# Kernel tuning notes

Hardware: AMD Instinct MI355X
Metric: run time of the kernel (lower is better)

Reference implementation:

```python
import jax, jax.numpy as jnp
import numpy as np

EPS = 1e-7
MAX_NORM = 1.0 - 1e-5  # Poincare ball (c=1) projection radius
NUM_NODES = 50000
NUM_EDGES = 800000
NUM_GRAPHS = 512
D_IN = 64
D_H = 64
D_OUT = 16


def _norm(x):
    return jnp.clip(jnp.linalg.norm(x, axis=-1, keepdims=True), EPS)


def expmap0(u):
    n = _norm(u)
    return jnp.tanh(n) * u / n


def logmap0(x):
    n = _norm(x)
    nc = jnp.clip(n, EPS, MAX_NORM)
    return jnp.arctanh(nc) * x / n


def proj(x):
    n = _norm(x)
    return jnp.where(n > MAX_NORM, x * (MAX_NORM / n), x)


def mobius_add(x, y):
    x2 = jnp.sum(x * x, axis=-1, keepdims=True)
    y2 = jnp.sum(y * y, axis=-1, keepdims=True)
    xy = jnp.sum(x * y, axis=-1, keepdims=True)
    num = (1.0 + 2.0 * xy + y2) * x + (1.0 - x2) * y
    den = jnp.clip(1.0 + 2.0 * xy + x2 * y2, EPS)
    return num / den


def hyp_linear(x, W, b):
    # mobius matvec + hyperbolic bias add
    h = proj(expmap0(logmap0(x) @ W.T))
    hb = proj(expmap0(b))
    return proj(mobius_add(h, hb))


def hyp_agg(x, src, dst, num_nodes):
    # mean aggregation of neighbor messages in the tangent space at the origin
    xt = logmap0(x)                                   # [N, d]
    msg = xt[src]                                     # [E, d] gather
    s = jax.ops.segment_sum(msg, dst, num_segments=num_nodes)
    cnt = jax.ops.segment_sum(jnp.ones((msg.shape[0],), xt.dtype), dst,
                              num_segments=num_nodes)
    agg = s / jnp.clip(cnt, 1.0)[:, None]
    return proj(expmap0(agg))


def hyp_act(x, act):
    return proj(expmap0(act(logmap0(x))))


def hgcn_layer(x, W, b, src, dst, num_nodes, act):
    h = hyp_linear(x, W, b)
    h = hyp_agg(h, src, dst, num_nodes)
    if act is not None:
        h = hyp_act(h, act)
    return h


def setup_inputs() -> dict:
    key = jax.random.key(0)
    ks = jax.random.split(key, 12)
    x = jax.random.normal(ks[0], (NUM_NODES, D_IN), jnp.float32) * 0.1
    edge_index = jax.random.randint(ks[1], (2, NUM_EDGES), 0, NUM_NODES, jnp.int64 if jax.config.jax_enable_x64 else jnp.int32)
    batch = jnp.sort(jax.random.randint(ks[2], (NUM_NODES,), 0, NUM_GRAPHS))
    def w(k, o, i):
        return jax.random.normal(k, (o, i), jnp.float32) * (1.0 / np.sqrt(i))
    return {
        "x": x,
        "W1": w(ks[3], D_H, D_IN), "b1": jnp.zeros((D_H,), jnp.float32),
        "W2": w(ks[4], D_H, D_H),  "b2": jnp.zeros((D_H,), jnp.float32),
        "W3": w(ks[5], D_H, D_H),  "b3": jnp.zeros((D_H,), jnp.float32),
        "W4": w(ks[6], D_OUT, D_H), "b4": jnp.zeros((D_OUT,), jnp.float32),
        "edge_index": edge_index,
        "batch": batch,
    }


def reference(x, W1, b1, W2, b2, W3, b3, W4, b4, edge_index, batch):
    act = lambda v: jax.nn.leaky_relu(v, 0.2)
    n = x.shape[0]
    src, dst = edge_index[0], edge_index[1]
    h = proj(expmap0(x))
    h = hgcn_layer(h, W1, b1, src, dst, n, act)
    h = hgcn_layer(h, W2, b2, src, dst, n, act)
    h = hgcn_layer(h, W3, b3, src, dst, n, None)
    t = logmap0(h)
    # global mean pool over graphs (eval-mode dropout = identity)
    s = jax.ops.segment_sum(t, batch, num_segments=NUM_GRAPHS)
    cnt = jax.ops.segment_sum(jnp.ones((n,), t.dtype), batch, num_segments=NUM_GRAPHS)
    pooled = s / jnp.clip(cnt, 1.0)[:, None]            # [G, d]
    h = proj(expmap0(pooled))
    out = hyp_linear(h, W4, b4)                          # HNNLayer, no activation
    return out
```

## Files before the change

### kernel.cpp

```cpp
#include <hip/hip_runtime.h>
#include <hip/hip_fp16.h>

#define EPSF 1e-7f
#define MAXNORM (1.0f - 1e-5f)

__device__ __forceinline__ float rsum64(float v) {
#pragma unroll
  for (int m = 32; m; m >>= 1) v += __shfl_xor(v, m, 64);
  return v;
}
__device__ __forceinline__ float rsum16(float v) {
#pragma unroll
  for (int m = 8; m; m >>= 1) v += __shfl_xor(v, m, 64);
  return v;
}
__device__ __forceinline__ float gr8(float v) {
  v += __shfl_xor(v, 1, 64);
  v += __shfl_xor(v, 2, 64);
  v += __shfl_xor(v, 4, 64);
  return v;
}

__device__ __forceinline__ float frcp(float x) { return __builtin_amdgcn_rcpf(x); }
__device__ __forceinline__ float fsqrt_(float x) { return __builtin_amdgcn_sqrtf(x); }
__device__ __forceinline__ float tanh_fast(float x) {
  x = fminf(x, 20.f);
  float e = __builtin_amdgcn_exp2f(x * 2.88539008178f);
  return (e - 1.f) * frcp(e + 1.f);
}
__device__ __forceinline__ float atanh_fast(float x) {
  return 0.34657359028f * __builtin_amdgcn_logf((1.f + x) * frcp(1.f - x));
}
__device__ __forceinline__ float lp_exp_log_scale(float nu) {
  float te = tanh_fast(nu);
  float tec = fminf(fmaxf(te, EPSF), MAXNORM);
  return atanh_fast(tec) * frcp(fmaxf(te, EPSF)) * te * frcp(nu);
}

__device__ __forceinline__ float4 ld4(const float* p) {
  return *reinterpret_cast<const float4*>(p);
}

__device__ __forceinline__ void gather8h(const unsigned short* __restrict__ csr,
                                         const __half* __restrict__ xtp,
                                         int r0, int deg, int g, int sub,
                                         float acc[8]) {
  const uint4* xt4 = reinterpret_cast<const uint4*>(xtp);
  for (int j0 = 0; j0 < deg; j0 += 8) {
    int myidx = 0;
    if (j0 + sub < deg) myidx = (int)csr[r0 + j0 + sub];
#pragma unroll
    for (int m = 0; m < 8; ++m) {
      int idx = __shfl(myidx, (g << 3) | m, 64);
      float msk = (j0 + m < deg) ? 1.f : 0.f;
      union { uint4 u; __half2 h[4]; } U;
      U.u = xt4[(size_t)idx * 8 + sub];
      float2 f0 = __half22float2(U.h[0]);
      float2 f1 = __half22float2(U.h[1]);
      float2 f2 = __half22float2(U.h[2]);
      float2 f3 = __half22float2(U.h[3]);
      acc[0] = fmaf(msk, f0.x, acc[0]); acc[1] = fmaf(msk, f0.y, acc[1]);
      acc[2] = fmaf(msk, f1.x, acc[2]); acc[3] = fmaf(msk, f1.y, acc[3]);
      acc[4] = fmaf(msk, f2.x, acc[4]); acc[5] = fmaf(msk, f2.y, acc[5]);
      acc[6] = fmaf(msk, f3.x, acc[6]); acc[7] = fmaf(msk, f3.y, acc[7]);
    }
  }
}

__device__ __forceinline__ void st8h(__half* __restrict__ xt, int node, int sub,
                                     const float o[8]) {
  union { uint4 u; __half2 h[4]; } U;
  U.h[0] = __floats2half2_rn(o[0], o[1]);
  U.h[1] = __floats2half2_rn(o[2], o[3]);
  U.h[2] = __floats2half2_rn(o[4], o[5]);
  U.h[3] = __floats2half2_rn(o[6], o[7]);
  reinterpret_cast<uint4*>(xt)[(size_t)node * 8 + sub] = U.u;
}

__device__ __forceinline__ void linear_tail8(
    const float* __restrict__ Wl, float* __restrict__ sc, int g, int sub,
    int lane, const float t2[8], const float hb8[8], float hb2, float out8[8]) {
  float4* sw = reinterpret_cast<float4*>(sc + g * 68 + sub * 8);
  sw[0] = make_float4(t2[0], t2[1], t2[2], t2[3]);
  sw[1] = make_float4(t2[4], t2[5], t2[6], t2[7]);
  float y[8] = {0.f, 0.f, 0.f, 0.f, 0.f, 0.f, 0.f, 0.f};
  const float4* Wrow = reinterpret_cast<const float4*>(Wl + lane * 68);
#pragma unroll
  for (int q = 0; q < 16; ++q) {
    float4 w = Wrow[q];
#pragma unroll
    for (int g2 = 0; g2 < 8; ++g2) {
      float4 tq = *reinterpret_cast<const float4*>(sc + g2 * 68 + q * 4);
      y[g2] = fmaf(w.x, tq.x, fmaf(w.y, tq.y, fmaf(w.z, tq.z, fmaf(w.w, tq.w, y[g2]))));
    }
  }
#pragma unroll
  for (int g2 = 0; g2 < 8; ++g2) sc[g2 * 68 + lane] = y[g2];
  float4 r0 = *reinterpret_cast<const float4*>(sc + g * 68 + sub * 8);
  float4 r1 = *reinterpret_cast<const float4*>(sc + g * 68 + sub * 8 + 4);
  float yv[8] = {r0.x, r0.y, r0.z, r0.w, r1.x, r1.y, r1.z, r1.w};
  float p1 = 0.f, p2 = 0.f;
#pragma unroll
  for (int j = 0; j < 8; ++j) {
    p1 = fmaf(yv[j], yv[j], p1);
    p2 = fmaf(yv[j], hb8[j], p2);
  }
  p1 = gr8(p1); p2 = gr8(p2);
  float ny = fmaxf(fsqrt_(p1), EPSF);
  float cy = fminf(tanh_fast(ny), MAXNORM);
  float k = cy * frcp(ny);
  float xy = k * p2;
  float x2 = cy * cy;
  float aa = 1.f + 2.f * xy + hb2;
  float cc = 1.f - x2;
  float den = fmaxf(1.f + 2.f * xy + x2 * hb2, EPSF);
  float rd = frcp(den);
  float nr2 = (aa * aa * x2 + 2.f * aa * cc * xy + cc * cc * hb2) * rd * rd;
  float nr = fmaxf(fsqrt_(nr2), EPSF);
  float s = atanh_fast(fminf(nr, MAXNORM)) * frcp(nr);
  float sk = s * rd;
#pragma unroll
  for (int j = 0; j < 8; ++j) out8[j] = sk * (aa * k * yv[j] + cc * hb8[j]);
}

__global__ void k_hist8(const int* __restrict__ dst, int* __restrict__ deg8,
                        int* __restrict__ rank, int E, int N) {
  int e = blockIdx.x * blockDim.x + threadIdx.x;
  if (e >= E) return;
  int c = blockIdx.x & 7;
  rank[e] = atomicAdd(&deg8[(size_t)c * N + dst[e]], 1);
}

__global__ void __launch_bounds__(256) k_red8(const int* __restrict__ deg8,
                                              int* __restrict__ offs8,
                                              int* __restrict__ deg, int N) {
  int d = blockIdx.x * blockDim.x + threadIdx.x;
  if (d >= N) return;
  int s = 0;
#pragma unroll
  for (int k = 0; k < 8; ++k) {
    int v = deg8[(size_t)k * N + d];
    offs8[(size_t)k * N + d] = s;
    s += v;
  }
  deg[d] = s;
}

__global__ void __launch_bounds__(256) k_scanA(const int* __restrict__ deg,
                                               int* __restrict__ locscan,
                                               int* __restrict__ partial, int N) {
  __shared__ int buf[256];
  int i = blockIdx.x * 256 + threadIdx.x;
  int v = (i < N) ? deg[i] : 0;
  buf[threadIdx.x] = v;
  __syncthreads();
#pragma unroll
  for (int off = 1; off < 256; off <<= 1) {
    int t = (threadIdx.x >= off) ? buf[threadIdx.x - off] : 0;
    __syncthreads();
    buf[threadIdx.x] += t;
    __syncthreads();
  }
  if (i < N) locscan[i] = buf[threadIdx.x] - v;
  if (threadIdx.x == 255) partial[blockIdx.x] = buf[255];
}

__global__ void __launch_bounds__(256) k_scanB(int* __restrict__ partial, int nb) {
  __shared__ int buf[256];
  int v = (threadIdx.x < nb) ? partial[threadIdx.x] : 0;
  buf[threadIdx.x] = v;
  __syncthreads();
#pragma unroll
  for (int off = 1; off < 256; off <<= 1) {
    int t = (threadIdx.x >= off) ? buf[threadIdx.x - off] : 0;
    __syncthreads();
    buf[threadIdx.x] += t;
    __syncthreads();
  }
  if (threadIdx.x < nb) partial[threadIdx.x] = buf[threadIdx.x] - v;
}

__global__ void __launch_bounds__(256) k_scanC(const int* __restrict__ locscan,
                                               const int* __restrict__ partial,
                                               int* __restrict__ rowptr, int N, int E) {
  int i = blockIdx.x * 256 + threadIdx.x;
  if (i < N) rowptr[i] = locscan[i] + partial[blockIdx.x];
  if (i == 0) rowptr[N] = E;
}

__global__ void k_fillnr(const int* __restrict__ src, const int* __restrict__ dst,
                         const int* __restrict__ rank,
                         const int* __restrict__ rowptr,
                         const int* __restrict__ offs8,
                         unsigned short* __restrict__ csr, int E, int N) {
  int e = blockIdx.x * blockDim.x + threadIdx.x;
  if (e >= E) return;
  int c = blockIdx.x & 7;
  int d = dst[e];
  csr[rowptr[d] + offs8[(size_t)c * N + d] + rank[e]] = (unsigned short)src[e];
}

__global__ void k_gsize(const int* __restrict__ batch, float* __restrict__ cntg,
                        int N, int G) {
  int g = blockIdx.x * blockDim.x + threadIdx.x;
  if (g >= G) return;
  int lo = 0, hi = N;
  while (lo < hi) { int mid = (lo + hi) >> 1; if (batch[mid] < g) lo = mid + 1; else hi = mid; }
  int lb = lo;
  lo = 0; hi = N; int g1 = g + 1;
  while (lo < hi) { int mid = (lo + hi) >> 1; if (batch[mid] < g1) lo = mid + 1; else hi = mid; }
  cntg[g] = (float)(lo - lb);
}

__global__ void __launch_bounds__(192) k_prepb(const float* __restrict__ b1,
                                               const float* __restrict__ b2,
                                               const float* __restrict__ b3,
                                               float* __restrict__ hb_all,
                                               float* __restrict__ hb2_all) {
  int w = threadIdx.x >> 6, lane = threadIdx.x & 63;
  const float* b = (w == 0) ? b1 : (w == 1) ? b2 : b3;
  float bb = b[lane];
  float nb = fmaxf(fsqrt_(rsum64(bb * bb)), EPSF);
  float tb = tanh_fast(nb);
  float cb = fminf(tb, MAXNORM);
  float hb = cb * frcp(nb) * bb;
  hb_all[w * 64 + lane] = hb;
  if (lane == 0) hb2_all[w] = cb * cb;
}

__global__ void __launch_bounds__(512) k_lin1(const float* __restrict__ x,
                                              const float* __restrict__ W,
                                              const float* __restrict__ hb,
                                              const float* __restrict__ hb2p,
                                              __half* __restrict__ xt, int N) {
  __shared__ __align__(16) float Wl[64 * 68];
  __shared__ __align__(16) float sc_all[8][8 * 68];
  int tid = threadIdx.x, wid = tid >> 6, lane = tid & 63;
  int g = lane >> 3, sub = lane & 7;
  for (int i = tid; i < 4096; i += 512) Wl[(i >> 6) * 68 + (i & 63)] = W[i];
  __syncthreads();
  float hb2 = hb2p[0];
  float4 h0 = ld4(hb + sub * 8), h1 = ld4(hb + sub * 8 + 4);
  float hb8[8] = {h0.x, h0.y, h0.z, h0.w, h1.x, h1.y, h1.z, h1.w};

  int slot = blockIdx.x * 64 + wid * 8 + g;
  bool valid = slot < N;
  int node = valid ? slot : 0;
  const float* row = x + (size_t)node * 64 + sub * 8;
  float4 v0 = ld4(row), v1 = ld4(row + 4);
  float xa[8] = {v0.x, v0.y, v0.z, v0.w, v1.x, v1.y, v1.z, v1.w};
  float p = 0.f;
#pragma unroll
  for (int j = 0; j < 8; ++j) p = fmaf(xa[j], xa[j], p);
  p = gr8(p);
  float na = fmaxf(fsqrt_(p), EPSF);
  float sc1 = lp_exp_log_scale(na);
  float t2[8];
#pragma unroll
  for (int j = 0; j < 8; ++j) t2[j] = sc1 * xa[j];
  float out8[8];
  linear_tail8(Wl, sc_all[wid], g, sub, lane, t2, hb8, hb2, out8);
  if (valid) st8h(xt, node, sub, out8);
}

__global__ void __launch_bounds__(512) k_gatherlin(
    const int* __restrict__ rowptr, const unsigned short* __restrict__ csr,
    const __half* __restrict__ xtp, const float* __restrict__ W,
    const float* __restrict__ hb, const float* __restrict__ hb2p,
    __half* __restrict__ xt, int N) {
  __shared__ __align__(16) float Wl[64 * 68];
  __shared__ __align__(16) float sc_all[8][8 * 68];
  int tid = threadIdx.x, wid = tid >> 6, lane = tid & 63;
  int g = lane >> 3, sub = lane & 7;
  for (int i = tid; i < 4096; i += 512) Wl[(i >> 6) * 68 + (i & 63)] = W[i];
  __syncthreads();
  float hb2 = hb2p[0];
  float4 h0 = ld4(hb + sub * 8), h1 = ld4(hb + sub * 8 + 4);
  float hb8[8] = {h0.x, h0.y, h0.z, h0.w, h1.x, h1.y, h1.z, h1.w};

  int slot = blockIdx.x * 64 + wid * 8 + g;
  bool valid = slot < N;
  int node = valid ? slot : 0;
  int r0 = rowptr[node];
  int deg = valid ? (rowptr[node + 1] - r0) : 0;
  float acc[8] = {0.f, 0.f, 0.f, 0.f, 0.f, 0.f, 0.f, 0.f};
  gather8h(csr, xtp, r0, deg, g, sub, acc);
  float rdeg = frcp(fmaxf((float)deg, 1.f));
  float u[8];
#pragma unroll
  for (int j = 0; j < 8; ++j) u[j] = acc[j] * rdeg;
  float p = 0.f, q = 0.f;
#pragma unroll
  for (int j = 0; j < 8; ++j) {
    float w = (u[j] < 0.f) ? 0.04f : 1.f;
    p = fmaf(u[j], u[j], p);
    q = fmaf(w * u[j], u[j], q);
  }
  p = gr8(p); q = gr8(q);
  float nu = fmaxf(fsqrt_(p), EPSF);
  float s1 = lp_exp_log_scale(nu);
  float nt = fmaxf(s1 * fsqrt_(q), EPSF);
  float f = lp_exp_log_scale(nt) * s1;
  float t2[8];
#pragma unroll
  for (int j = 0; j < 8; ++j) t2[j] = f * u[j] * ((u[j] < 0.f) ? 0.2f : 1.f);
  float out8[8];
  linear_tail8(Wl, sc_all[wid], g, sub, lane, t2, hb8, hb2, out8);
  if (valid) st8h(xt, node, sub, out8);
}

__global__ void __launch_bounds__(512) k_gpool(const int* __restrict__ rowptr,
                                               const unsigned short* __restrict__ csr,
                                               const __half* __restrict__ xtp,
                                               const int* __restrict__ batch,
                                               float* __restrict__ pooled, int N) {
  int tid = threadIdx.x, wid = tid >> 6, lane = tid & 63;
  int g = lane >> 3, sub = lane & 7;
  int slot = blockIdx.x * 64 + wid * 8 + g;
  bool valid = slot < N;
  int node = valid ? slot : 0;
  int r0 = rowptr[node];
  int deg = valid ? (rowptr[node + 1] - r0) : 0;
  float acc[8] = {0.f, 0.f, 0.f, 0.f, 0.f, 0.f, 0.f, 0.f};
  gather8h(csr, xtp, r0, deg, g, sub, acc);
  float rdeg = frcp(fmaxf((float)deg, 1.f));
  float u[8], p = 0.f;
#pragma unroll
  for (int j = 0; j < 8; ++j) {
    u[j] = acc[j] * rdeg;
    p = fmaf(u[j], u[j], p);
  }
  p = gr8(p);
  float nu = fmaxf(fsqrt_(p), EPSF);
  float s = lp_exp_log_scale(nu);
  float t8[8];
#pragma unroll
  for (int j = 0; j < 8; ++j) t8[j] = (valid ? s : 0.f) * u[j];
  int bs = batch[node];
  int b0 = __shfl(bs, 0, 64);
  bool uniform = __all(valid && bs == b0);
  if (uniform) {
#pragma unroll
    for (int j = 0; j < 8; ++j) {
      t8[j] += __shfl_xor(t8[j], 8, 64);
      t8[j] += __shfl_xor(t8[j], 16, 64);
      t8[j] += __shfl_xor(t8[j], 32, 64);
    }
    if (g == 0) {
#pragma unroll
      for (int j = 0; j < 8; ++j)
        atomicAdd(&pooled[(size_t)b0 * 64 + sub * 8 + j], t8[j]);
    }
  } else if (valid) {
#pragma unroll
    for (int j = 0; j < 8; ++j)
      atomicAdd(&pooled[(size_t)bs * 64 + sub * 8 + j], t8[j]);
  }
}

__global__ void __launch_bounds__(64) k_final(const float* __restrict__ pooled,
                                              const float* __restrict__ cntg,
                                              const float* __restrict__ W4,
                                              const float* __restrict__ b4,
                                              float* __restrict__ out, int G) {
  int g = blockIdx.x;
  int lane = threadIdx.x;
  float u = pooled[(size_t)g * 64 + lane] / fmaxf(cntg[g], 1.0f);
  float n = fmaxf(sqrtf(rsum64(u * u)), EPSF);
  float e = tanhf(n) * u / n;
  float ne = fmaxf(sqrtf(rsum64(e * e)), EPSF);
  if (ne > MAXNORM) e *= MAXNORM / ne;
  float nn = fmaxf(sqrtf(rsum64(e * e)), EPSF);
  float t = atanhf(fminf(nn, MAXNORM)) * e / nn;

  int row = lane & 15;
  float acc = 0.f;
#pragma unroll
  for (int k = 0; k < 64; ++k) {
    float tk = __shfl(t, k, 64);
    acc = fmaf(W4[row * 64 + k], tk, acc);
  }
  float ny = fmaxf(sqrtf(rsum16(acc * acc)), EPSF);
  float hy = tanhf(ny) * acc / ny;
  float nh = fmaxf(sqrtf(rsum16(hy * hy)), EPSF);
  if (nh > MAXNORM) hy *= MAXNORM / nh;
  float bb = b4[row];
  float nb = fmaxf(sqrtf(rsum16(bb * bb)), EPSF);
  float hb = tanhf(nb) * bb / nb;
  float nhb = fmaxf(sqrtf(rsum16(hb * hb)), EPSF);
  if (nhb > MAXNORM) hb *= MAXNORM / nhb;
  float x2 = rsum16(hy * hy);
  float y2 = rsum16(hb * hb);
  float xy = rsum16(hy * hb);
  float num = (1.f + 2.f * xy + y2) * hy + (1.f - x2) * hb;
  float den = fmaxf(1.f + 2.f * xy + x2 * y2, EPSF);
  float r = num / den;
  float nr = fmaxf(sqrtf(rsum16(r * r)), EPSF);
  if (nr > MAXNORM) r *= MAXNORM / nr;
  if (lane < 16) out[(size_t)g * 16 + lane] = r;
}

extern "C" void kernel_launch(void* const* d_in, const int* in_sizes, int n_in,
                              void* d_out, int out_size, void* d_ws, size_t ws_size,
                              hipStream_t stream) {
  const float* x  = (const float*)d_in[0];
  const float* W1 = (const float*)d_in[1];
  const float* b1 = (const float*)d_in[2];
  const float* W2 = (const float*)d_in[3];
  const float* b2 = (const float*)d_in[4];
  const float* W3 = (const float*)d_in[5];
  const float* b3 = (const float*)d_in[6];
  const float* W4 = (const float*)d_in[7];
  const float* b4 = (const float*)d_in[8];
  const int* ei   = (const int*)d_in[9];
  const int* batch = (const int*)d_in[10];

  int N = in_sizes[0] / 64;
  int E = in_sizes[9] / 2;
  int G = out_size / 16;
  const int* src = ei;
  const int* dst = ei + E;

  float* ws = (float*)d_ws;
  __half* xtA   = (__half*)ws;
  __half* xtB   = xtA + (size_t)N * 64;
  float* pooled = ws + (size_t)N * 64;
  float* cntg   = pooled + (size_t)G * 64;
  float* hb_all = cntg + G;
  float* hb2_all = hb_all + 192;
  int* ip       = (int*)(hb2_all + 4);
  int* deg8     = ip;
  int* offs8    = deg8 + (size_t)8 * N;
  int* deg      = offs8 + (size_t)8 * N;
  int* locscan  = deg + N;
  int* rowptr   = locscan + N;
  int* partial  = rowptr + N + 1;
  int* rank     = partial + 256;
  unsigned short* csr = (unsigned short*)(rank + E);
  float* out = (float*)d_out;

  int nbN = (N + 255) / 256;
  int nbE = (E + 255) / 256;
  int nb64 = (N + 63) / 64;

  hipMemsetAsync(deg8, 0, (size_t)8 * N * sizeof(int), stream);
  hipMemsetAsync(pooled, 0, (size_t)G * 64 * sizeof(float), stream);

  k_hist8<<<nbE, 256, 0, stream>>>(dst, deg8, rank, E, N);
  k_gsize<<<(G + 255) / 256, 256, 0, stream>>>(batch, cntg, N, G);
  k_red8<<<nbN, 256, 0, stream>>>(deg8, offs8, deg, N);
  k_scanA<<<nbN, 256, 0, stream>>>(deg, locscan, partial, N);
  k_scanB<<<1, 256, 0, stream>>>(partial, nbN);
  k_scanC<<<nbN, 256, 0, stream>>>(locscan, partial, rowptr, N, E);
  k_fillnr<<<nbE, 256, 0, stream>>>(src, dst, rank, rowptr, offs8, csr, E, N);

  k_prepb<<<1, 192, 0, stream>>>(b1, b2, b3, hb_all, hb2_all);

  k_lin1<<<nb64, 512, 0, stream>>>(x, W1, hb_all, hb2_all, xtA, N);
  k_gatherlin<<<nb64, 512, 0, stream>>>(rowptr, csr, xtA, W2, hb_all + 64,
                                        hb2_all + 1, xtB, N);
  k_gatherlin<<<nb64, 512, 0, stream>>>(rowptr, csr, xtB, W3, hb_all + 128,
                                        hb2_all + 2, xtA, N);
  k_gpool<<<nb64, 512, 0, stream>>>(rowptr, csr, xtA, batch, pooled, N);
  k_final<<<G, 64, 0, stream>>>(pooled, cntg, W4, b4, out, G);
}
```

Measured before the change: 185.0 us.

## Merge preprocessing kernels and compute bias in-kernel to cut launch count

Fuses the histogram with the graph-size kernel, the deg8 reduction with the local scan, and the CSR fill with the first linear layer into single launches split by block index. The separate bias-prep kernel is removed and each block now computes the hyperbolic bias itself. The CSR gather also prefetches the next batch of neighbor indices before processing the current one. This targets launch overhead and serialization across about 13 small kernels, at the cost of some repeated bias math per block and a multi-pass scanB loop.

```diff
diff --git a/kernel.cpp b/kernel.cpp
--- a/kernel.cpp
+++ b/kernel.cpp
@@ -41,17 +41,35 @@
   return *reinterpret_cast<const float4*>(p);
 }
 
+__device__ __forceinline__ void hb_from_b(const float* __restrict__ b, int sub,
+                                          float hb8[8], float& hb2) {
+  float4 b0 = ld4(b + sub * 8), b1 = ld4(b + sub * 8 + 4);
+  float bb8[8] = {b0.x, b0.y, b0.z, b0.w, b1.x, b1.y, b1.z, b1.w};
+  float p = 0.f;
+#pragma unroll
+  for (int j = 0; j < 8; ++j) p = fmaf(bb8[j], bb8[j], p);
+  p = gr8(p);
+  float nb = fmaxf(fsqrt_(p), EPSF);
+  float cb = fminf(tanh_fast(nb), MAXNORM);
+  float kb = cb * frcp(nb);
+#pragma unroll
+  for (int j = 0; j < 8; ++j) hb8[j] = kb * bb8[j];
+  hb2 = cb * cb;
+}
+
 __device__ __forceinline__ void gather8h(const unsigned short* __restrict__ csr,
                                          const __half* __restrict__ xtp,
                                          int r0, int deg, int g, int sub,
                                          float acc[8]) {
   const uint4* xt4 = reinterpret_cast<const uint4*>(xtp);
+  int lb = g << 3;
+  int cur = (sub < deg) ? (int)csr[r0 + sub] : 0;
   for (int j0 = 0; j0 < deg; j0 += 8) {
-    int myidx = 0;
-    if (j0 + sub < deg) myidx = (int)csr[r0 + j0 + sub];
+    int nj = j0 + 8;
+    int nxt = (nj + sub < deg) ? (int)csr[r0 + nj + sub] : 0;
 #pragma unroll
     for (int m = 0; m < 8; ++m) {
-      int idx = __shfl(myidx, (g << 3) | m, 64);
+      int idx = __shfl(cur, lb + m, 64);
       float msk = (j0 + m < deg) ? 1.f : 0.f;
       union { uint4 u; __half2 h[4]; } U;
       U.u = xt4[(size_t)idx * 8 + sub];
@@ -64,6 +82,7 @@
       acc[4] = fmaf(msk, f2.x, acc[4]); acc[5] = fmaf(msk, f2.y, acc[5]);
       acc[6] = fmaf(msk, f3.x, acc[6]); acc[7] = fmaf(msk, f3.y, acc[7]);
     }
+    cur = nxt;
   }
 }
 
@@ -123,36 +142,44 @@
   for (int j = 0; j < 8; ++j) out8[j] = sk * (aa * k * yv[j] + cc * hb8[j]);
 }
 
-__global__ void k_hist8(const int* __restrict__ dst, int* __restrict__ deg8,
-                        int* __restrict__ rank, int E, int N) {
-  int e = blockIdx.x * blockDim.x + threadIdx.x;
-  if (e >= E) return;
-  int c = blockIdx.x & 7;
-  rank[e] = atomicAdd(&deg8[(size_t)c * N + dst[e]], 1);
-}
-
-__global__ void __launch_bounds__(256) k_red8(const int* __restrict__ deg8,
-                                              int* __restrict__ offs8,
-                                              int* __restrict__ deg, int N) {
-  int d = blockIdx.x * blockDim.x + threadIdx.x;
-  if (d >= N) return;
-  int s = 0;
-#pragma unroll
-  for (int k = 0; k < 8; ++k) {
-    int v = deg8[(size_t)k * N + d];
-    offs8[(size_t)k * N + d] = s;
-    s += v;
-  }
-  deg[d] = s;
-}
-
-__global__ void __launch_bounds__(256) k_scanA(const int* __restrict__ deg,
-                                               int* __restrict__ locscan,
-                                               int* __restrict__ partial, int N) {
+__global__ void __launch_bounds__(256) k_histg(
+    const int* __restrict__ dst, int* __restrict__ deg8, int* __restrict__ rank,
+    int E, int N, const int* __restrict__ batch, float* __restrict__ cntg,
+    int G, int nbE) {
+  if ((int)blockIdx.x < nbE) {
+    int e = blockIdx.x * 256 + threadIdx.x;
+    if (e >= E) return;
+    int c = (e >> 8) & 7;
+    rank[e] = atomicAdd(&deg8[(size_t)c * N + dst[e]], 1);
+  } else {
+    int g = (blockIdx.x - nbE) * 256 + threadIdx.x;
+    if (g >= G) return;
+    int lo = 0, hi = N;
+    while (lo < hi) { int mid = (lo + hi) >> 1; if (batch[mid] < g) lo = mid + 1; else hi = mid; }
+    int lb = lo;
+    lo = 0; hi = N; int g1 = g + 1;
+    while (lo < hi) { int mid = (lo + hi) >> 1; if (batch[mid] < g1) lo = mid + 1; else hi = mid; }
+    cntg[g] = (float)(lo - lb);
+  }
+}
+
+__global__ void __launch_bounds__(256) k_scanAR(const int* __restrict__ deg8,
+                                                int* __restrict__ offs8,
+                                                int* __restrict__ locscan,
+                                                int* __restrict__ partial, int N) {
   __shared__ int buf[256];
   int i = blockIdx.x * 256 + threadIdx.x;
-  int v = (i < N) ? deg[i] : 0;
-  buf[threadIdx.x] = v;
+  int s = 0;
+  if (i < N) {
+#pragma unroll
+    for (int k = 0; k < 8; ++k) {
+      int v = deg8[(size_t)k * N + i];
+      offs8[(size_t)k * N + i] = s;
+      s += v;
+    }
+  }
+  int v0 = s;
+  buf[threadIdx.x] = v0;
   __syncthreads();
 #pragma unroll
   for (int off = 1; off < 256; off <<= 1) {
@@ -161,23 +188,30 @@
     buf[threadIdx.x] += t;
     __syncthreads();
   }
-  if (i < N) locscan[i] = buf[threadIdx.x] - v;
+  if (i < N) locscan[i] = buf[threadIdx.x] - v0;
   if (threadIdx.x == 255) partial[blockIdx.x] = buf[255];
 }
 
 __global__ void __launch_bounds__(256) k_scanB(int* __restrict__ partial, int nb) {
   __shared__ int buf[256];
-  int v = (threadIdx.x < nb) ? partial[threadIdx.x] : 0;
-  buf[threadIdx.x] = v;
-  __syncthreads();
-#pragma unroll
-  for (int off = 1; off < 256; off <<= 1) {
-    int t = (threadIdx.x >= off) ? buf[threadIdx.x - off] : 0;
+  int carry = 0;
+  for (int base = 0; base < nb; base += 256) {
+    int i = base + threadIdx.x;
+    int v = (i < nb) ? partial[i] : 0;
+    buf[threadIdx.x] = v;
     __syncthreads();
-    buf[threadIdx.x] += t;
+#pragma unroll
+    for (int off = 1; off < 256; off <<= 1) {
+      int t = (threadIdx.x >= off) ? buf[threadIdx.x - off] : 0;
+      __syncthreads();
+      buf[threadIdx.x] += t;
+      __syncthreads();
+    }
+    if (i < nb) partial[i] = carry + buf[threadIdx.x] - v;
+    int total = buf[255];
     __syncthreads();
-  }
-  if (threadIdx.x < nb) partial[threadIdx.x] = buf[threadIdx.x] - v;
+    carry += total;
+  }
 }
 
 __global__ void __launch_bounds__(256) k_scanC(const int* __restrict__ locscan,
@@ -188,95 +222,63 @@
   if (i == 0) rowptr[N] = E;
 }
 
-__global__ void k_fillnr(const int* __restrict__ src, const int* __restrict__ dst,
-                         const int* __restrict__ rank,
-                         const int* __restrict__ rowptr,
-                         const int* __restrict__ offs8,
-                         unsigned short* __restrict__ csr, int E, int N) {
-  int e = blockIdx.x * blockDim.x + threadIdx.x;
-  if (e >= E) return;
-  int c = blockIdx.x & 7;
-  int d = dst[e];
-  csr[rowptr[d] + offs8[(size_t)c * N + d] + rank[e]] = (unsigned short)src[e];
-}
-
-__global__ void k_gsize(const int* __restrict__ batch, float* __restrict__ cntg,
-                        int N, int G) {
-  int g = blockIdx.x * blockDim.x + threadIdx.x;
-  if (g >= G) return;
-  int lo = 0, hi = N;
-  while (lo < hi) { int mid = (lo + hi) >> 1; if (batch[mid] < g) lo = mid + 1; else hi = mid; }
-  int lb = lo;
-  lo = 0; hi = N; int g1 = g + 1;
-  while (lo < hi) { int mid = (lo + hi) >> 1; if (batch[mid] < g1) lo = mid + 1; else hi = mid; }
-  cntg[g] = (float)(lo - lb);
-}
-
-__global__ void __launch_bounds__(192) k_prepb(const float* __restrict__ b1,
-                                               const float* __restrict__ b2,
-                                               const float* __restrict__ b3,
-                                               float* __restrict__ hb_all,
-                                               float* __restrict__ hb2_all) {
-  int w = threadIdx.x >> 6, lane = threadIdx.x & 63;
-  const float* b = (w == 0) ? b1 : (w == 1) ? b2 : b3;
-  float bb = b[lane];
-  float nb = fmaxf(fsqrt_(rsum64(bb * bb)), EPSF);
-  float tb = tanh_fast(nb);
-  float cb = fminf(tb, MAXNORM);
-  float hb = cb * frcp(nb) * bb;
-  hb_all[w * 64 + lane] = hb;
-  if (lane == 0) hb2_all[w] = cb * cb;
-}
-
-__global__ void __launch_bounds__(512) k_lin1(const float* __restrict__ x,
-                                              const float* __restrict__ W,
-                                              const float* __restrict__ hb,
-                                              const float* __restrict__ hb2p,
-                                              __half* __restrict__ xt, int N) {
+__global__ void __launch_bounds__(512) k_filllin(
+    const int* __restrict__ src, const int* __restrict__ dst,
+    const int* __restrict__ rank, const int* __restrict__ rowptr,
+    const int* __restrict__ offs8, unsigned short* __restrict__ csr,
+    int E, int N, int nbF,
+    const float* __restrict__ x, const float* __restrict__ W,
+    const float* __restrict__ b, __half* __restrict__ xt) {
+  __shared__ __align__(16) float Wl[64 * 68];
+  __shared__ __align__(16) float sc_all[8][8 * 68];
+  if ((int)blockIdx.x < nbF) {
+    int e = blockIdx.x * 512 + threadIdx.x;
+    if (e >= E) return;
+    int c = (e >> 8) & 7;
+    int d = dst[e];
+    csr[rowptr[d] + offs8[(size_t)c * N + d] + rank[e]] = (unsigned short)src[e];
+    return;
+  }
+  int bb = blockIdx.x - nbF;
+  int tid = threadIdx.x, wid = tid >> 6, lane = tid & 63;
+  int g = lane >> 3, sub = lane & 7;
+  for (int i = tid; i < 4096; i += 512) Wl[(i >> 6) * 68 + (i & 63)] = W[i];
+  __syncthreads();
+  float hb8[8], hb2;
+  hb_from_b(b, sub, hb8, hb2);
+
+  int slot = bb * 64 + wid * 8 + g;
+  bool valid = slot < N;
+  int node = valid ? slot : 0;
+  const float* row = x + (size_t)node * 64 + sub * 8;
+  float4 v0 = ld4(row), v1 = ld4(row + 4);
+  float xa[8] = {v0.x, v0.y, v0.z, v0.w, v1.x, v1.y, v1.z, v1.w};
+  float p = 0.f;
+#pragma unroll
+  for (int j = 0; j < 8; ++j) p = fmaf(xa[j], xa[j], p);
+  p = gr8(p);
+  float na = fmaxf(fsqrt_(p), EPSF);
+  float sc1 = lp_exp_log_scale(na);
+  float t2[8];
+#pragma unroll
+  for (int j = 0; j < 8; ++j) t2[j] = sc1 * xa[j];
+  float out8[8];
+  linear_tail8(Wl, sc_all[wid], g, sub, lane, t2, hb8, hb2, out8);
+  if (valid) st8h(xt, node, sub, out8);
+}
+
+__global__ void __launch_bounds__(512) k_gatherlin(
+    const int* __restrict__ rowptr, const unsigned short* __restrict__ csr,
+    const __half* __restrict__ xtp, const float* __restrict__ W,
+    const float* __restrict__ b, __half* __restrict__ xt, int N) {
   __shared__ __align__(16) float Wl[64 * 68];
   __shared__ __align__(16) float sc_all[8][8 * 68];
   int tid = threadIdx.x, wid = tid >> 6, lane = tid & 63;
   int g = lane >> 3, sub = lane & 7;
   for (int i = tid; i < 4096; i += 512) Wl[(i >> 6) * 68 + (i & 63)] = W[i];
   __syncthreads();
-  float hb2 = hb2p[0];
-  float4 h0 = ld4(hb + sub * 8), h1 = ld4(hb + sub * 8 + 4);
-  float hb8[8] = {h0.x, h0.y, h0.z, h0.w, h1.x, h1.y, h1.z, h1.w};
-
-  int slot = blockIdx.x * 64 + wid * 8 + g;
-  bool valid = slot < N;
-  int node = valid ? slot : 0;
-  const float* row = x + (size_t)node * 64 + sub * 8;
-  float4 v0 = ld4(row), v1 = ld4(row + 4);
-  float xa[8] = {v0.x, v0.y, v0.z, v0.w, v1.x, v1.y, v1.z, v1.w};
-  float p = 0.f;
-#pragma unroll
-  for (int j = 0; j < 8; ++j) p = fmaf(xa[j], xa[j], p);
-  p = gr8(p);
-  float na = fmaxf(fsqrt_(p), EPSF);
-  float sc1 = lp_exp_log_scale(na);
-  float t2[8];
-#pragma unroll
-  for (int j = 0; j < 8; ++j) t2[j] = sc1 * xa[j];
-  float out8[8];
-  linear_tail8(Wl, sc_all[wid], g, sub, lane, t2, hb8, hb2, out8);
-  if (valid) st8h(xt, node, sub, out8);
-}
-
-__global__ void __launch_bounds__(512) k_gatherlin(
-    const int* __restrict__ rowptr, const unsigned short* __restrict__ csr,
-    const __half* __restrict__ xtp, const float* __restrict__ W,
-    const float* __restrict__ hb, const float* __restrict__ hb2p,
-    __half* __restrict__ xt, int N) {
-  __shared__ __align__(16) float Wl[64 * 68];
-  __shared__ __align__(16) float sc_all[8][8 * 68];
-  int tid = threadIdx.x, wid = tid >> 6, lane = tid & 63;
-  int g = lane >> 3, sub = lane & 7;
-  for (int i = tid; i < 4096; i += 512) Wl[(i >> 6) * 68 + (i & 63)] = W[i];
-  __syncthreads();
-  float hb2 = hb2p[0];
-  float4 h0 = ld4(hb + sub * 8), h1 = ld4(hb + sub * 8 + 4);
-  float hb8[8] = {h0.x, h0.y, h0.z, h0.w, h1.x, h1.y, h1.z, h1.w};
+  float hb8[8], hb2;
+  hb_from_b(b, sub, hb8, hb2);
 
   int slot = blockIdx.x * 64 + wid * 8 + g;
   bool valid = slot < N;
@@ -426,41 +428,33 @@
   __half* xtB   = xtA + (size_t)N * 64;
   float* pooled = ws + (size_t)N * 64;
   float* cntg   = pooled + (size_t)G * 64;
-  float* hb_all = cntg + G;
-  float* hb2_all = hb_all + 192;
-  int* ip       = (int*)(hb2_all + 4);
+  int* ip       = (int*)(cntg + G);
   int* deg8     = ip;
   int* offs8    = deg8 + (size_t)8 * N;
-  int* deg      = offs8 + (size_t)8 * N;
-  int* locscan  = deg + N;
+  int* locscan  = offs8 + (size_t)8 * N;
   int* rowptr   = locscan + N;
   int* partial  = rowptr + N + 1;
   int* rank     = partial + 256;
   unsigned short* csr = (unsigned short*)(rank + E);
   float* out = (float*)d_out;
 
+  int nbE = (E + 255) / 256;
+  int nbG = (G + 255) / 256;
   int nbN = (N + 255) / 256;
-  int nbE = (E + 255) / 256;
-  int nb64 = (N + 63) / 64;
+  int nbF = (E + 511) / 512;
+  int nbL = (N + 63) / 64;
 
   hipMemsetAsync(deg8, 0, (size_t)8 * N * sizeof(int), stream);
   hipMemsetAsync(pooled, 0, (size_t)G * 64 * sizeof(float), stream);
 
-  k_hist8<<<nbE, 256, 0, stream>>>(dst, deg8, rank, E, N);
-  k_gsize<<<(G + 255) / 256, 256, 0, stream>>>(batch, cntg, N, G);
-  k_red8<<<nbN, 256, 0, stream>>>(deg8, offs8, deg, N);
-  k_scanA<<<nbN, 256, 0, stream>>>(deg, locscan, partial, N);
+  k_histg<<<nbE + nbG, 256, 0, stream>>>(dst, deg8, rank, E, N, batch, cntg, G, nbE);
+  k_scanAR<<<nbN, 256, 0, stream>>>(deg8, offs8, locscan, partial, N);
   k_scanB<<<1, 256, 0, stream>>>(partial, nbN);
   k_scanC<<<nbN, 256, 0, stream>>>(locscan, partial, rowptr, N, E);
-  k_fillnr<<<nbE, 256, 0, stream>>>(src, dst, rank, rowptr, offs8, csr, E, N);
-
-  k_prepb<<<1, 192, 0, stream>>>(b1, b2, b3, hb_all, hb2_all);
-
-  k_lin1<<<nb64, 512, 0, stream>>>(x, W1, hb_all, hb2_all, xtA, N);
-  k_gatherlin<<<nb64, 512, 0, stream>>>(rowptr, csr, xtA, W2, hb_all + 64,
-                                        hb2_all + 1, xtB, N);
-  k_gatherlin<<<nb64, 512, 0, stream>>>(rowptr, csr, xtB, W3, hb_all + 128,
-                                        hb2_all + 2, xtA, N);
-  k_gpool<<<nb64, 512, 0, stream>>>(rowptr, csr, xtA, batch, pooled, N);
+  k_filllin<<<nbF + nbL, 512, 0, stream>>>(src, dst, rank, rowptr, offs8, csr,
+                                           E, N, nbF, x, W1, b1, xtA);
+  k_gatherlin<<<nbL, 512, 0, stream>>>(rowptr, csr, xtA, W2, b2, xtB, N);
+  k_gatherlin<<<nbL, 512, 0, stream>>>(rowptr, csr, xtB, W3, b3, xtA, N);
+  k_gpool<<<nbL, 512, 0, stream>>>(rowptr, csr, xtA, batch, pooled, N);
   k_final<<<G, 64, 0, stream>>>(pooled, cntg, W4, b4, out, G);
 }
```

Result: faster. 174.3 us (median of 2 runs) (-5.8%).
